# Optimization experiments

Hardware: AMD Instinct MI355X
Metric: run time of the kernel (lower is better)

The kernel has to match this reference:

```python
import jax, jax.numpy as jnp
import numpy as np


def setup_inputs() -> dict:
    key = jax.random.key(0)
    k1, k2, k3 = jax.random.split(key, 3)
    B, D, H, W = 16, 1024, 16, 16
    num_codebooks, K = 1, 8192
    d_head = D // num_codebooks
    x = jax.random.normal(k1, (B, D, H, W), dtype=jnp.float32)
    codebook = jax.random.normal(k2, (num_codebooks, K, d_head), dtype=jnp.float32)
    values = jax.random.normal(k3, (num_codebooks, K, d_head), dtype=jnp.float32)
    return {"x": x, "codebook": codebook, "values": values}


def reference(x, codebook, values):
    # x: [B, D, H, W] feature map; codebook/values: [h, K, d] with h*d == D
    B, D, H, W = x.shape
    h, K, d = codebook.shape
    N = H * W
    # (B, D, H, W) -> (B, N, D) -> (B, N, h, d): per-head token embeddings
    tokens = x.reshape(B, D, N).transpose(0, 2, 1).reshape(B, N, h, d)
    # Squared L2 distance to each code: ||t||^2 - 2 t.e + ||e||^2
    t_sq = jnp.sum(tokens * tokens, axis=-1, keepdims=True)          # [B,N,h,1]
    e_sq = jnp.sum(codebook * codebook, axis=-1)                     # [h,K]
    cross = jnp.einsum("bnhd,hkd->bnhk", tokens, codebook)          # [B,N,h,K]
    dist = t_sq - 2.0 * cross + e_sq[None, None, :, :]               # [B,N,h,K]
    idx = jnp.argmin(dist, axis=-1)                                  # [B,N,h]
    # Gather value memories per head: values[head, idx]
    head_ids = jnp.arange(h)[None, None, :]                          # [1,1,h]
    memories = values[head_ids, idx]                                 # [B,N,h,d]
    # (B, N, h*d) -> (B, D, N) -> (B, D, H, W)
    out = memories.reshape(B, N, D).transpose(0, 2, 1).reshape(B, D, H, W)
    return out
```

## Files before the change

### kernel.cpp

```cpp
#include <hip/hip_runtime.h>
#include <cstdint>


constexpr int Dd = 1024;
constexpr int Nn = 256;
constexpr int Bb = 16;
constexpr int Kk = 8192;
constexpr int Mm = 4096;
constexpr int STAGES = Dd / 64;
constexpr int NITER = STAGES / 2;
constexpr int NCHUNK = Kk / 64;
constexpr int NCAND = NCHUNK * 2;
constexpr float QS = 24.0f;
constexpr float SC2 = 2.0f / (QS * QS);

typedef __attribute__((ext_vector_type(4))) int vi4;
typedef unsigned long long u64;
typedef unsigned char uchar;

__device__ __forceinline__ void gload16(const void* g, void* l) {
    __builtin_amdgcn_global_load_lds((const __attribute__((address_space(1))) uint32_t*)g,
                                     (__attribute__((address_space(3))) uint32_t*)l, 16, 0, 0);
}

template <int CTRL>
__device__ __forceinline__ uint32_t rot16(uint32_t v) {
    return (uint32_t)__builtin_amdgcn_update_dpp(0, (int)v, CTRL, 0xF, 0xF, true);
}
template <int CTRL>
__device__ __forceinline__ u64 rot16_64(u64 v) {
    uint32_t lo = rot16<CTRL>((uint32_t)v);
    uint32_t hi = rot16<CTRL>((uint32_t)(v >> 32));
    return ((u64)hi << 32) | lo;
}

__device__ __forceinline__ void mm2u(uint32_t& a, uint32_t& b) {
    uint32_t lo = a < b ? a : b;
    uint32_t hi = a < b ? b : a;
    a = lo; b = hi;
}
__device__ __forceinline__ void merge2u(uint32_t& a1, uint32_t& a2, uint32_t b1,
                                        uint32_t b2) {
    uint32_t t1 = a1 < b1 ? a1 : b1;
    uint32_t hi = a1 < b1 ? b1 : a1;
    uint32_t l2 = a2 < b2 ? a2 : b2;
    a2 = hi < l2 ? hi : l2;
    a1 = t1;
}

__device__ __forceinline__ int q8(float v) {
    int qi = (int)rintf(v * QS);
    qi = qi > 127 ? 127 : (qi < -127 ? -127 : qi);
    return qi & 0xFF;
}
__device__ __forceinline__ int pk4i(float a, float b, float c, float d) {
    return q8(a) | (q8(b) << 8) | (q8(c) << 16) | (q8(d) << 24);
}


__global__ __launch_bounds__(256) void prep_kernel(const float* __restrict__ x,
                                                   const float* __restrict__ cb,
                                                   uchar* __restrict__ Apk,
                                                   uchar* __restrict__ Bpk,
                                                   float* __restrict__ esq,
                                                   float* __restrict__ xT) {
    const int tid = threadIdx.x;
    if (blockIdx.x < 512) {
        const int rl = tid >> 4, seg = tid & 15;
        const int code = blockIdx.x * 16 + rl;
        const float* src = cb + (size_t)code * Dd + seg * 64;
        float v[64];
        float ss = 0.f;
#pragma unroll
        for (int j = 0; j < 64; j += 4) {
            float4 f = *(const float4*)&src[j];
            v[j] = f.x; v[j + 1] = f.y; v[j + 2] = f.z; v[j + 3] = f.w;
            ss += f.x * f.x + f.y * f.y + f.z * f.z + f.w * f.w;
        }
#pragma unroll
        for (int off = 8; off; off >>= 1) ss += __shfl_down(ss, off, 16);
        if (seg == 0) esq[code] = ss;
        const int g = code >> 4, rlane = code & 15;
#pragma unroll
        for (int q = 0; q < 4; ++q) {
            int o[4];
#pragma unroll
            for (int w4 = 0; w4 < 4; ++w4) {
                const int j = q * 16 + w4 * 4;
                o[w4] = pk4i(v[j], v[j + 1], v[j + 2], v[j + 3]);
            }
            *(uint4*)&Bpk[((size_t)(g * 16 + seg) * 64 + (rlane | (q << 4))) * 16] =
                *(const uint4*)o;
        }
    } else {
        const int bb = blockIdx.x - 512;
        const int b = bb >> 5, d0 = (bb & 31) * 32, n = tid;
        const int t = b * 256 + n;
        const float* xb = x + (size_t)b * Dd * Nn + n;
        const int g = t >> 4, rlane = t & 15, kb = d0 >> 6, qbase = (d0 & 32) >> 4;
        float v[32];
#pragma unroll
        for (int jj = 0; jj < 32; ++jj) v[jj] = xb[(size_t)(d0 + jj) * Nn];
#pragma unroll
        for (int h = 0; h < 2; ++h) {
            int o[4];
#pragma unroll
            for (int w4 = 0; w4 < 4; ++w4) {
                const int j = h * 16 + w4 * 4;
                o[w4] = pk4i(v[j], v[j + 1], v[j + 2], v[j + 3]);
            }
            *(uint4*)&Apk[((size_t)(g * 16 + kb) * 64 + (rlane | ((qbase + h) << 4))) * 16] =
                *(const uint4*)o;
        }
        if (xT) {
            float* row = xT + (size_t)t * Dd + d0;
#pragma unroll
            for (int jj = 0; jj < 32; jj += 4) {
                float4 f;
                f.x = v[jj]; f.y = v[jj + 1]; f.z = v[jj + 2]; f.w = v[jj + 3];
                *(float4*)&row[jj] = f;
            }
        }
    }
}

__global__ __launch_bounds__(256) void transx_kernel(const float* __restrict__ x,
                                                     float* __restrict__ xT) {
    const int n = threadIdx.x, b = blockIdx.x, d0 = blockIdx.y * 32;
    const float* xb = x + (size_t)b * Dd * Nn + n;
    float* row = xT + (size_t)(b * Nn + n) * Dd + d0;
#pragma unroll
    for (int jj = 0; jj < 8; ++jj) {
        float4 v;
        v.x = xb[(size_t)(d0 + jj * 4 + 0) * Nn];
        v.y = xb[(size_t)(d0 + jj * 4 + 1) * Nn];
        v.z = xb[(size_t)(d0 + jj * 4 + 2) * Nn];
        v.w = xb[(size_t)(d0 + jj * 4 + 3) * Nn];
        *(float4*)&row[jj * 4] = v;
    }
}

__global__ __launch_bounds__(512, 2) void mfma_dist_kernel(const uchar* __restrict__ Apk,
                                                           const uchar* __restrict__ Bpk,
                                                           const float* __restrict__ esq,
                                                           u64* __restrict__ cand) {
    __shared__ uchar As[2 * 2 * 16 * 1024];
    __shared__ uchar Bs[2 * 2 * 16 * 1024];

    const int tid = threadIdx.x, lane = tid & 63, w = tid >> 6;
    const int wm = w >> 2, wn = w & 3;
    const int nBase = blockIdx.x * 256, mBase = blockIdx.y * 256;
    const int gA = blockIdx.y * 16, gB = blockIdx.x * 16;

    vi4 acc[8][4];
#pragma unroll
    for (int i = 0; i < 8; ++i)
#pragma unroll
        for (int j = 0; j < 4; ++j) acc[i][j] = (vi4)0;

    const uchar* gmat = (w < 4) ? Apk : Bpk;
    const int gBase = ((w < 4) ? gA : gB) + (w & 3) * 4;
    const uchar* gsrc = gmat + (size_t)gBase * 16384 + (size_t)lane * 16;
    uchar* swave = ((w < 4) ? As : Bs) + (w & 3) * 4096;

    auto stage_iter = [&](int buf, int it) {
#pragma unroll
        for (int kt = 0; kt < 2; ++kt) {
            const int kb = 2 * it + kt;
            uchar* ldst = swave + buf * 32768 + kt * 16384;
#pragma unroll
            for (int r = 0; r < 4; ++r)
                gload16(gsrc + (size_t)(r * 16 + kb) * 1024, ldst + r * 1024);
        }
    };

    auto compute = [&](int buf, int kt) {
        const uchar* ab = As + buf * 32768 + kt * 16384;
        const uchar* bb = Bs + buf * 32768 + kt * 16384;
        vi4 af[8], bf[4];
#pragma unroll
        for (int mi = 0; mi < 8; ++mi)
            af[mi] = *(const vi4*)&ab[((wm * 8 + mi) * 64 + lane) * 16];
#pragma unroll
        for (int ni = 0; ni < 4; ++ni)
            bf[ni] = *(const vi4*)&bb[((wn * 4 + ni) * 64 + lane) * 16];
#pragma unroll
        for (int mi = 0; mi < 8; ++mi)
#pragma unroll
            for (int ni = 0; ni < 4; ++ni)
                acc[mi][ni] = __builtin_amdgcn_mfma_i32_16x16x64_i8(
                    af[mi], bf[ni], acc[mi][ni], 0, 0, 0);
    };

    stage_iter(0, 0);

    for (int i = 0; i < NITER; ++i) {
        const int buf = i & 1;
        asm volatile("s_waitcnt vmcnt(0)" ::: "memory");
        __builtin_amdgcn_s_barrier();
        __builtin_amdgcn_sched_barrier(0);
        if (i + 1 < NITER) stage_iter(buf ^ 1, i + 1);
        __builtin_amdgcn_s_setprio(1);
        compute(buf, 0);
        compute(buf, 1);
        __builtin_amdgcn_s_setprio(0);
    }

    const int chunk = blockIdx.x * 4 + wn;
    const uint32_t cbase = (uint32_t)(nBase + wn * 64);
    float e4[4];
#pragma unroll
    for (int ni = 0; ni < 4; ++ni) e4[ni] = esq[cbase + ni * 16 + (lane & 15)];
#pragma unroll
    for (int mi = 0; mi < 8; ++mi) {
#pragma unroll
        for (int reg = 0; reg < 4; ++reg) {
            uint32_t p[4];
#pragma unroll
            for (int ni = 0; ni < 4; ++ni) {
                float s = fmaxf(fmaf(-SC2, (float)acc[mi][ni][reg], e4[ni]), 0.f);
                p[ni] = (__float_as_uint(s) & 0xFFFFFFC0u) |
                        (uint32_t)(ni * 16 + (lane & 15));
            }
            mm2u(p[0], p[1]); mm2u(p[2], p[3]);
            merge2u(p[0], p[1], p[2], p[3]);
            uint32_t t1 = p[0], t2 = p[1];
            { uint32_t o1 = rot16<0x121>(t1), o2 = rot16<0x121>(t2);
              merge2u(t1, t2, o1, o2); }
            { uint32_t o1 = rot16<0x122>(t1), o2 = rot16<0x122>(t2);
              merge2u(t1, t2, o1, o2); }
            { uint32_t o1 = rot16<0x124>(t1), o2 = rot16<0x124>(t2);
              merge2u(t1, t2, o1, o2); }
            { uint32_t o1 = rot16<0x128>(t1), o2 = rot16<0x128>(t2);
              merge2u(t1, t2, o1, o2); }
            if ((lane & 15) == 0) {
                const int t = mBase + wm * 128 + mi * 16 + (lane >> 4) * 4 + reg;
                cand[(size_t)t * NCAND + chunk * 2 + 0] =
                    ((u64)(t1 & 0xFFFFFFC0u) << 32) | (cbase + (t1 & 63u));
                cand[(size_t)t * NCAND + chunk * 2 + 1] =
                    ((u64)(t2 & 0xFFFFFFC0u) << 32) | (cbase + (t2 & 63u));
            }
        }
    }
}

__global__ __launch_bounds__(256) void selres_kernel(const u64* __restrict__ cand,
                                                     const float* __restrict__ xT,
                                                     const float* __restrict__ cb,
                                                     const float* __restrict__ esq,
                                                     int* __restrict__ fidx) {
    __shared__ u64 wtop[4][4];
    __shared__ int cs[4];
    __shared__ float red[4][4];
    const int t = blockIdx.x, tid = threadIdx.x, lane = tid & 63, w = tid >> 6;
    u64 v = cand[(size_t)t * NCAND + tid];
#pragma unroll
    for (int rd = 0; rd < 4; ++rd) {
        u64 m = v;
        { u64 o = rot16_64<0x121>(m); m = m < o ? m : o; }
        { u64 o = rot16_64<0x122>(m); m = m < o ? m : o; }
        { u64 o = rot16_64<0x124>(m); m = m < o ? m : o; }
        { u64 o = rot16_64<0x128>(m); m = m < o ? m : o; }
        { u64 o = __shfl_xor(m, 16, 64); m = m < o ? m : o; }
        { u64 o = __shfl_xor(m, 32, 64); m = m < o ? m : o; }
        if (lane == 0) wtop[w][rd] = m;
        if (v == m) v = ~0ULL;
    }
    __syncthreads();
    if (tid == 0) {
        u64 a[16];
#pragma unroll
        for (int i = 0; i < 16; ++i) a[i] = wtop[i >> 2][i & 3];
#pragma unroll
        for (int rd = 0; rd < 4; ++rd) {
            int bi = 0;
            u64 m = a[0];
#pragma unroll
            for (int i = 1; i < 16; ++i)
                if (a[i] < m) { m = a[i]; bi = i; }
            cs[rd] = (int)(uint32_t)m;
            a[bi] = ~0ULL;
        }
    }
    __syncthreads();
    int c[4];
#pragma unroll
    for (int j = 0; j < 4; ++j) c[j] = cs[j];
    float4 xv = *(const float4*)&xT[(size_t)t * Dd + tid * 4];
    float part[4];
#pragma unroll
    for (int cc = 0; cc < 4; ++cc) {
        float4 wv = *(const float4*)&cb[(size_t)c[cc] * Dd + tid * 4];
        part[cc] = xv.x * wv.x + xv.y * wv.y + xv.z * wv.z + xv.w * wv.w;
    }
#pragma unroll
    for (int cc = 0; cc < 4; ++cc)
#pragma unroll
        for (int off = 32; off; off >>= 1) part[cc] += __shfl_down(part[cc], off, 64);
    if ((tid & 63) == 0)
#pragma unroll
        for (int cc = 0; cc < 4; ++cc) red[tid >> 6][cc] = part[cc];
    __syncthreads();
    if (tid == 0) {
        float bs = 1e30f;
        int bi = 0x7FFFFFFF;
#pragma unroll
        for (int cc = 0; cc < 4; ++cc) {
            float cross = red[0][cc] + red[1][cc] + red[2][cc] + red[3][cc];
            float s = fmaf(-2.f, cross, esq[c[cc]]);
            if (s < bs || (s == bs && c[cc] < bi)) { bs = s; bi = c[cc]; }
        }
        fidx[t] = bi;
    }
}

__global__ __launch_bounds__(256) void gather_kernel(const int* __restrict__ fidx,
                                                     const float* __restrict__ values,
                                                     float* __restrict__ out) {
    const int n = threadIdx.x, b = blockIdx.x, dc = blockIdx.y;
    const int row = fidx[b * Nn + n];
    const float* src = values + (size_t)row * Dd + dc * 64;
    float* dst = out + (size_t)b * Dd * Nn + (size_t)dc * 64 * Nn + n;
#pragma unroll
    for (int j = 0; j < 64; j += 4) {
        float4 v = *(const float4*)(src + j);
        dst[(j + 0) * Nn] = v.x;
        dst[(j + 1) * Nn] = v.y;
        dst[(j + 2) * Nn] = v.z;
        dst[(j + 3) * Nn] = v.w;
    }
}

extern "C" void kernel_launch(void* const* d_in, const int* in_sizes, int n_in,
                              void* d_out, int out_size, void* d_ws, size_t ws_size,
                              hipStream_t stream) {
    const float* x = (const float*)d_in[0];
    const float* cb = (const float*)d_in[1];
    const float* vals = (const float*)d_in[2];
    float* out = (float*)d_out;

    char* p = (char*)d_ws;
    uchar* Apk = (uchar*)p;
    uchar* Bpk = (uchar*)(p + ((size_t)4 << 20));
    float* esq = (float*)(p + ((size_t)16 << 20));
    u64* cand = (u64*)(p + ((size_t)16 << 20) + Kk * 4);
    int* fidx = (int*)(p + ((size_t)16 << 20) + Kk * 4 + (size_t)Mm * NCAND * 8);
    const size_t base = ((size_t)16 << 20) + Kk * 4 + (size_t)Mm * NCAND * 8 + Mm * 4;
    const bool bigws = ws_size >= base + ((size_t)16 << 20);
    float* xT = bigws ? (float*)(p + base) : (float*)d_ws;

    prep_kernel<<<1024, 256, 0, stream>>>(x, cb, Apk, Bpk, esq,
                                          bigws ? xT : nullptr);
    mfma_dist_kernel<<<dim3(32, 16), 512, 0, stream>>>(Apk, Bpk, esq, cand);
    if (!bigws) transx_kernel<<<dim3(Bb, 32), 256, 0, stream>>>(x, xT);
    selres_kernel<<<Mm, 256, 0, stream>>>(cand, xT, cb, esq, fidx);
    gather_kernel<<<dim3(Bb, Dd / 64), 256, 0, stream>>>(fidx, vals, out);
}
```

Before: 174.7 us.

## Process one token per wavefront in selection/rescoring kernel, removing block syncs

The selection and exact-rescoring kernel now assigns one token to each wavefront, with eight tokens per 512-thread block, instead of one token per 256-thread block. Each lane holds four candidates and does the top-4 selection with wave-level reductions only, so the shared-memory staging, the serial single-thread merge and the block barriers are gone. The dot products for the rescoring are accumulated over four strided slices per lane and reduced with xor shuffles. Each lane now does more serial work and holds more registers, and far fewer blocks are launched.

Result: faster. 170.9 us (-2.2%).

```diff
diff --git a/kernel.cpp b/kernel.cpp
--- a/kernel.cpp
+++ b/kernel.cpp
@@ -244,71 +244,57 @@
     }
 }
 
-__global__ __launch_bounds__(256) void selres_kernel(const u64* __restrict__ cand,
+__global__ __launch_bounds__(512) void selres_kernel(const u64* __restrict__ cand,
                                                      const float* __restrict__ xT,
                                                      const float* __restrict__ cb,
                                                      const float* __restrict__ esq,
                                                      int* __restrict__ fidx) {
-    __shared__ u64 wtop[4][4];
-    __shared__ int cs[4];
-    __shared__ float red[4][4];
-    const int t = blockIdx.x, tid = threadIdx.x, lane = tid & 63, w = tid >> 6;
-    u64 v = cand[(size_t)t * NCAND + tid];
+    const int tid = threadIdx.x, lane = tid & 63, w = tid >> 6;
+    const int t = blockIdx.x * 8 + w;
+    const u64* cp = cand + (size_t)t * NCAND;
+    u64 c0 = cp[lane], c1 = cp[lane + 64], c2 = cp[lane + 128], c3 = cp[lane + 192];
+    int cs[4];
 #pragma unroll
     for (int rd = 0; rd < 4; ++rd) {
-        u64 m = v;
+        u64 a01 = c0 < c1 ? c0 : c1;
+        u64 a23 = c2 < c3 ? c2 : c3;
+        u64 m = a01 < a23 ? a01 : a23;
         { u64 o = rot16_64<0x121>(m); m = m < o ? m : o; }
         { u64 o = rot16_64<0x122>(m); m = m < o ? m : o; }
         { u64 o = rot16_64<0x124>(m); m = m < o ? m : o; }
         { u64 o = rot16_64<0x128>(m); m = m < o ? m : o; }
         { u64 o = __shfl_xor(m, 16, 64); m = m < o ? m : o; }
         { u64 o = __shfl_xor(m, 32, 64); m = m < o ? m : o; }
-        if (lane == 0) wtop[w][rd] = m;
-        if (v == m) v = ~0ULL;
-    }
-    __syncthreads();
-    if (tid == 0) {
-        u64 a[16];
-#pragma unroll
-        for (int i = 0; i < 16; ++i) a[i] = wtop[i >> 2][i & 3];
-#pragma unroll
-        for (int rd = 0; rd < 4; ++rd) {
-            int bi = 0;
-            u64 m = a[0];
-#pragma unroll
-            for (int i = 1; i < 16; ++i)
-                if (a[i] < m) { m = a[i]; bi = i; }
-            cs[rd] = (int)(uint32_t)m;
-            a[bi] = ~0ULL;
-        }
-    }
-    __syncthreads();
-    int c[4];
-#pragma unroll
-    for (int j = 0; j < 4; ++j) c[j] = cs[j];
-    float4 xv = *(const float4*)&xT[(size_t)t * Dd + tid * 4];
-    float part[4];
-#pragma unroll
-    for (int cc = 0; cc < 4; ++cc) {
-        float4 wv = *(const float4*)&cb[(size_t)c[cc] * Dd + tid * 4];
-        part[cc] = xv.x * wv.x + xv.y * wv.y + xv.z * wv.z + xv.w * wv.w;
+        cs[rd] = (int)(uint32_t)m;
+        if (c0 == m) c0 = ~0ULL;
+        else if (c1 == m) c1 = ~0ULL;
+        else if (c2 == m) c2 = ~0ULL;
+        else if (c3 == m) c3 = ~0ULL;
+    }
+    const float* xrow = xT + (size_t)t * Dd;
+    float part[4] = {0.f, 0.f, 0.f, 0.f};
+#pragma unroll
+    for (int jj = 0; jj < 4; ++jj) {
+        const int off = jj * 256 + lane * 4;
+        float4 xv = *(const float4*)&xrow[off];
+#pragma unroll
+        for (int cc = 0; cc < 4; ++cc) {
+            float4 wv = *(const float4*)&cb[(size_t)cs[cc] * Dd + off];
+            part[cc] += xv.x * wv.x + xv.y * wv.y + xv.z * wv.z + xv.w * wv.w;
+        }
     }
 #pragma unroll
     for (int cc = 0; cc < 4; ++cc)
 #pragma unroll
-        for (int off = 32; off; off >>= 1) part[cc] += __shfl_down(part[cc], off, 64);
-    if ((tid & 63) == 0)
-#pragma unroll
-        for (int cc = 0; cc < 4; ++cc) red[tid >> 6][cc] = part[cc];
-    __syncthreads();
-    if (tid == 0) {
+        for (int off = 1; off < 64; off <<= 1)
+            part[cc] += __shfl_xor(part[cc], off, 64);
+    if (lane == 0) {
         float bs = 1e30f;
         int bi = 0x7FFFFFFF;
 #pragma unroll
         for (int cc = 0; cc < 4; ++cc) {
-            float cross = red[0][cc] + red[1][cc] + red[2][cc] + red[3][cc];
-            float s = fmaf(-2.f, cross, esq[c[cc]]);
-            if (s < bs || (s == bs && c[cc] < bi)) { bs = s; bi = c[cc]; }
+            float s = fmaf(-2.f, part[cc], esq[cs[cc]]);
+            if (s < bs || (s == bs && cs[cc] < bi)) { bs = s; bi = cs[cc]; }
         }
         fidx[t] = bi;
     }
@@ -353,6 +339,6 @@
                                           bigws ? xT : nullptr);
     mfma_dist_kernel<<<dim3(32, 16), 512, 0, stream>>>(Apk, Bpk, esq, cand);
     if (!bigws) transx_kernel<<<dim3(Bb, 32), 256, 0, stream>>>(x, xT);
-    selres_kernel<<<Mm, 256, 0, stream>>>(cand, xT, cb, esq, fidx);
+    selres_kernel<<<Mm / 8, 512, 0, stream>>>(cand, xT, cb, esq, fidx);
     gather_kernel<<<dim3(Bb, Dd / 64), 256, 0, stream>>>(fidx, vals, out);
 }
```
